# Performance work log

Measured on AMD Instinct MI355X. Metric: run time of the kernel, lower is better.

## Reference

```python
import jax, jax.numpy as jnp
import numpy as np

N = 100000          # num nodes
E = 3200000         # num edges (avg degree 32)
CLIN = 64           # clinical feature dim
MEL_SHAPE = (32, 40)  # flattened -> 1280
MEL = 1280
H = 128             # hidden_dim
C = 4               # num_classes


def setup_inputs() -> dict:
    key = jax.random.key(0)
    ks = jax.random.split(key, 14)
    s = lambda d: 1.0 / np.sqrt(d)
    inp = {
        "clinical": jax.random.normal(ks[0], (N, CLIN), jnp.float32),
        "mel": jax.random.normal(ks[1], (N,) + MEL_SHAPE, jnp.float32),
        "edge_index": jax.random.randint(ks[2], (2, E), 0, N, dtype=jnp.int32),
        # mel_linear
        "Wm": jax.random.normal(ks[3], (H, MEL), jnp.float32) * s(MEL),
        "bm": jnp.zeros((H,), jnp.float32),
        # concat_linear (in = H + CLIN)
        "Wc": jax.random.normal(ks[4], (H, H + CLIN), jnp.float32) * s(H + CLIN),
        "bc": jnp.zeros((H,), jnp.float32),
        # sage1: lin_l (neighbors, with bias), lin_r (root, no bias)
        "Wl1": jax.random.normal(ks[5], (H, H), jnp.float32) * s(H),
        "bl1": jnp.zeros((H,), jnp.float32),
        "Wr1": jax.random.normal(ks[6], (H, H), jnp.float32) * s(H),
        # sage2
        "Wl2": jax.random.normal(ks[7], (C, H), jnp.float32) * s(H),
        "bl2": jnp.zeros((C,), jnp.float32),
        "Wr2": jax.random.normal(ks[8], (C, H), jnp.float32) * s(H),
    }
    return inp


def _sage_conv(x, src, dst, Wl, bl, Wr):
    """PyG SAGEConv with mean aggregation:
    out = lin_l(mean_{j in N(i)} x_j) + lin_r(x_i).
    src = edge_index[0] (message source), dst = edge_index[1] (target).
    """
    msg_sum = jax.ops.segment_sum(x[src], dst, num_segments=N)  # [N, d]
    cnt = jax.ops.segment_sum(jnp.ones((src.shape[0], 1), x.dtype), dst,
                              num_segments=N)                    # [N, 1]
    agg = msg_sum / jnp.maximum(cnt, 1.0)
    return agg @ Wl.T + bl + x @ Wr.T


def reference(clinical, mel, edge_index, Wm, bm, Wc, bc,
              Wl1, bl1, Wr1, Wl2, bl2, Wr2):
    src, dst = edge_index[0], edge_index[1]
    mel_flat = mel.reshape(mel.shape[0], -1)                 # [N, 1280]
    mel_h = jax.nn.relu(mel_flat @ Wm.T + bm)                # [N, H]
    x = jnp.concatenate([clinical, mel_h], axis=1)           # [N, CLIN+H]
    x = jax.nn.relu(x @ Wc.T + bc)                           # [N, H]
    x = jax.nn.relu(_sage_conv(x, src, dst, Wl1, bl1, Wr1))  # [N, H]
    x = _sage_conv(x, src, dst, Wl2, bl2, Wr2)               # [N, C]
    return x
```

## Files before the change

### kernel.cpp

```cpp
#include <hip/hip_runtime.h>
#include <hip/hip_bf16.h>
#include <stdint.h>

#define NN   100000
#define EE   3200000
#define HD   128

typedef short v8s __attribute__((ext_vector_type(8)));
typedef float v4f __attribute__((ext_vector_type(4)));

__device__ __forceinline__ unsigned short f2bf(float f){
  union { float f; unsigned int i; } v; v.f = f;
  unsigned int r = v.i + 0x7fffu + ((v.i >> 16) & 1u);
  return (unsigned short)(r >> 16);
}
__device__ __forceinline__ uint4 pack8(float4 lo, float4 hi){
  uint4 r;
  r.x = (unsigned)f2bf(lo.x) | ((unsigned)f2bf(lo.y) << 16);
  r.y = (unsigned)f2bf(lo.z) | ((unsigned)f2bf(lo.w) << 16);
  r.z = (unsigned)f2bf(hi.x) | ((unsigned)f2bf(hi.y) << 16);
  r.w = (unsigned)f2bf(hi.z) | ((unsigned)f2bf(hi.w) << 16);
  return r;
}

__global__ void k_zero(int* p, int n){
  int i = blockIdx.x*blockDim.x + threadIdx.x; if (i < n) p[i] = 0;
}
__global__ void k_histrank(const int* __restrict__ dst, int* __restrict__ cnt,
                           int* __restrict__ rank, int e){
  int i = blockIdx.x*blockDim.x + threadIdx.x;
  if (i < e) rank[i] = atomicAdd(&cnt[dst[i]], 1);
}
__global__ __launch_bounds__(1024)
void k_scan1(const int* __restrict__ cnt, int* __restrict__ offs, int* __restrict__ blksum, int n){
  __shared__ int lds[1024];
  int t = threadIdx.x; int i = blockIdx.x*1024 + t;
  int v = (i < n) ? cnt[i] : 0;
  lds[t] = v; __syncthreads();
  for (int s = 1; s < 1024; s <<= 1){
    int add = (t >= s) ? lds[t-s] : 0;
    __syncthreads();
    lds[t] += add;
    __syncthreads();
  }
  if (i < n) offs[i] = lds[t] - v;
  if (t == 1023) blksum[blockIdx.x] = lds[1023];
}
__global__ __launch_bounds__(128)
void k_scan2(int* __restrict__ blksum, int nb){
  __shared__ int lds[128];
  int t = threadIdx.x;
  int v = (t < nb) ? blksum[t] : 0;
  lds[t] = v; __syncthreads();
  for (int s = 1; s < 128; s <<= 1){
    int a = (t >= s) ? lds[t-s] : 0;
    __syncthreads();
    lds[t] += a;
    __syncthreads();
  }
  if (t < nb) blksum[t] = lds[t] - v;
}
__global__ __launch_bounds__(1024)
void k_scan3(int* __restrict__ offs, const int* __restrict__ blksum, int n){
  int i = blockIdx.x*1024 + threadIdx.x;
  if (i < n) offs[i] += blksum[blockIdx.x];
}
__global__ void k_place(const int* __restrict__ src, const int* __restrict__ dst,
                        const int* __restrict__ offs, const int* __restrict__ rank,
                        int* __restrict__ ssrc, int e){
  int i = blockIdx.x*blockDim.x + threadIdx.x;
  if (i < e) ssrc[offs[dst[i]] + rank[i]] = src[i];
}

__device__ __forceinline__ void gemm_issue(int t, int T0, int M, int gm, int r0, int c8,
    const void* __restrict__ A0, int lda0, int a0f32,
    const void* __restrict__ A1, int lda1, int a1f32,
    const float* __restrict__ B0, int ldb0,
    const float* __restrict__ B1, int ldb1,
    uint4* as, uint4* bs)
{
  const void* Ag; const float* Bg; int la, lb, ko, af32;
  if (t < T0){ Ag = A0; la = lda0; af32 = a0f32; Bg = B0; lb = ldb0; ko = t*64; }
  else       { Ag = A1; la = lda1; af32 = a1f32; Bg = B1; lb = ldb1; ko = (t-T0)*64; }
#pragma unroll
  for (int p = 0; p < 4; p++){
    int row  = r0 + p*32;
    int grow = gm + row;
    if (grow < M){
      if (af32){
        const float* ap = (const float*)Ag + (size_t)grow*la + ko + c8;
        as[p] = pack8(*(const float4*)ap, *(const float4*)(ap + 4));
      } else {
        as[p] = *(const uint4*)((const unsigned short*)Ag + (size_t)grow*la + ko + c8);
      }
    } else {
      as[p] = make_uint4(0u,0u,0u,0u);
    }
    const float* bp = Bg + (size_t)row*lb + ko + c8;
    bs[p] = pack8(*(const float4*)bp, *(const float4*)(bp + 4));
  }
}

__global__ __launch_bounds__(256)
void k_gemm(int M,
            const void* __restrict__ A0, int lda0, int K0, int a0f32,
            const void* __restrict__ A1, int lda1, int K1, int a1f32,
            const float* __restrict__ B0, int ldb0,
            const float* __restrict__ B1, int ldb1,
            const float* __restrict__ bias, int do_relu,
            unsigned short* __restrict__ C, int ldc)
{
  __shared__ unsigned short Abuf[128*72];
  __shared__ unsigned short Bbuf[128*72];
  const int tid = threadIdx.x;
  const int gm  = blockIdx.x * 128;
  const int T0  = K0 >> 6;
  const int T   = (K0 + K1) >> 6;

  const int r0 = tid >> 3;
  const int c8 = (tid & 7) * 8;

  const int lane = tid & 63;
  const int w  = tid >> 6;
  const int wm = w >> 1, wn = w & 1;
  const int l15 = lane & 15, q = lane >> 4;

  v4f acc[4][4];
#pragma unroll
  for (int mi = 0; mi < 4; mi++)
#pragma unroll
    for (int ni = 0; ni < 4; ni++){ v4f z = {0.f,0.f,0.f,0.f}; acc[mi][ni] = z; }

  uint4 aS[4], bS[4];
  gemm_issue(0, T0, M, gm, r0, c8, A0, lda0, a0f32, A1, lda1, a1f32,
             B0, ldb0, B1, ldb1, aS, bS);

  for (int t = 0; t < T; ++t){
#pragma unroll
    for (int p = 0; p < 4; p++){
      int row = r0 + p*32;
      *(uint4*)(Abuf + row*72 + c8) = aS[p];
      *(uint4*)(Bbuf + row*72 + c8) = bS[p];
    }
    __syncthreads();
    if (t + 1 < T)
      gemm_issue(t+1, T0, M, gm, r0, c8, A0, lda0, a0f32, A1, lda1, a1f32,
                 B0, ldb0, B1, ldb1, aS, bS);
#pragma unroll
    for (int kk = 0; kk < 64; kk += 32){
      v8s af[4], bf[4];
#pragma unroll
      for (int mi = 0; mi < 4; mi++)
        af[mi] = *(const v8s*)(Abuf + (wm*64 + mi*16 + l15)*72 + kk + q*8);
#pragma unroll
      for (int ni = 0; ni < 4; ni++)
        bf[ni] = *(const v8s*)(Bbuf + (wn*64 + ni*16 + l15)*72 + kk + q*8);
#pragma unroll
      for (int mi = 0; mi < 4; mi++)
#pragma unroll
        for (int ni = 0; ni < 4; ni++)
          acc[mi][ni] = __builtin_amdgcn_mfma_f32_16x16x32_bf16(af[mi], bf[ni], acc[mi][ni], 0, 0, 0);
    }
    __syncthreads();
  }

#pragma unroll
  for (int ni = 0; ni < 4; ni++){
    int n = wn*64 + ni*16 + l15;
    float bv = bias ? bias[n] : 0.0f;
#pragma unroll
    for (int mi = 0; mi < 4; mi++){
#pragma unroll
      for (int r = 0; r < 4; r++){
        int row = gm + wm*64 + mi*16 + q*4 + r;
        if (row < M){
          float v = acc[mi][ni][r] + bv;
          if (do_relu) v = v > 0.f ? v : 0.f;
          C[(size_t)row*ldc + n] = f2bf(v);
        }
      }
    }
  }
}

__global__ __launch_bounds__(256)
void k_agg1(const int* __restrict__ offs, const int* __restrict__ cnt,
            const int* __restrict__ ssrc,
            const unsigned short* __restrict__ y1,
            const unsigned short* __restrict__ z1,
            const float* __restrict__ Wl2,
            const float* __restrict__ Wr2,
            const float* __restrict__ bl2,
            float* __restrict__ y2, float* __restrict__ r2, int n)
{
  int wid  = (blockIdx.x * blockDim.x + threadIdx.x) >> 6;
  int lane = threadIdx.x & 63;
  if (wid >= n) return;
  int start = offs[wid];
  int deg   = cnt[wid];
  const unsigned int* y1u = (const unsigned int*)y1;
  float a0 = 0.f, a1 = 0.f;
  for (int base = 0; base < deg; base += 64){
    int idx = base + lane;
    int sl  = (idx < deg) ? ssrc[start + idx] : 0;
    int m   = deg - base; if (m > 64) m = 64;
    for (int t = 0; t < m; ++t){
      int s = __shfl(sl, t, 64);
      unsigned int u = y1u[(size_t)s*64 + lane];
      union {unsigned int i; float f;} lo, hi;
      lo.i = u << 16; hi.i = u & 0xffff0000u;
      a0 += lo.f; a1 += hi.f;
    }
  }
  float scale = 1.0f / (float)(deg > 0 ? deg : 1);
  unsigned int zu = ((const unsigned int*)z1)[(size_t)wid*64 + lane];
  union {unsigned int i; float f;} zl, zh;
  zl.i = zu << 16; zh.i = zu & 0xffff0000u;
  float x0 = a0*scale + zl.f; x0 = x0 > 0.f ? x0 : 0.f;
  float x1 = a1*scale + zh.f; x1 = x1 > 0.f ? x1 : 0.f;

  float pl[4], pr[4];
#pragma unroll
  for (int c = 0; c < 4; c++){
    float2 wl = ((const float2*)Wl2)[c*64 + lane];
    float2 wr = ((const float2*)Wr2)[c*64 + lane];
    pl[c] = x0*wl.x + x1*wl.y;
    pr[c] = x0*wr.x + x1*wr.y;
  }
#pragma unroll
  for (int off = 32; off > 0; off >>= 1){
#pragma unroll
    for (int c = 0; c < 4; c++){
      pl[c] += __shfl_xor(pl[c], off, 64);
      pr[c] += __shfl_xor(pr[c], off, 64);
    }
  }
  if (lane < 4){
    y2[(size_t)wid*4 + lane] = pl[lane];
    r2[(size_t)wid*4 + lane] = pr[lane] + bl2[lane];
  }
}

__global__ void k_agg2(const int* __restrict__ offs, const int* __restrict__ cnt,
                       const int* __restrict__ ssrc,
                       const float* __restrict__ y2, const float* __restrict__ r2,
                       float* __restrict__ out, int n)
{
  int i = blockIdx.x * blockDim.x + threadIdx.x;
  if (i >= n) return;
  int start = offs[i], deg = cnt[i];
  float a0 = 0.f, a1 = 0.f, a2 = 0.f, a3 = 0.f;
  for (int e = 0; e < deg; e++){
    int s = ssrc[start + e];
    float4 v = *(const float4*)(y2 + (size_t)s*4);
    a0 += v.x; a1 += v.y; a2 += v.z; a3 += v.w;
  }
  float sc = 1.0f / (float)(deg > 0 ? deg : 1);
  float4 r = *(const float4*)(r2 + (size_t)i*4);
  float4 o;
  o.x = a0*sc + r.x; o.y = a1*sc + r.y; o.z = a2*sc + r.z; o.w = a3*sc + r.w;
  *(float4*)(out + (size_t)i*4) = o;
}

extern "C" void kernel_launch(void* const* d_in, const int* in_sizes, int n_in,
                              void* d_out, int out_size, void* d_ws, size_t ws_size,
                              hipStream_t stream)
{
  (void)in_sizes; (void)n_in; (void)out_size; (void)ws_size;
  const float* clinical = (const float*)d_in[0];
  const float* mel      = (const float*)d_in[1];
  const int*   ei       = (const int*)d_in[2];
  const float* Wm  = (const float*)d_in[3];
  const float* bm  = (const float*)d_in[4];
  const float* Wc  = (const float*)d_in[5];
  const float* bc  = (const float*)d_in[6];
  const float* Wl1 = (const float*)d_in[7];
  const float* bl1 = (const float*)d_in[8];
  const float* Wr1 = (const float*)d_in[9];
  const float* Wl2 = (const float*)d_in[10];
  const float* bl2 = (const float*)d_in[11];
  const float* Wr2 = (const float*)d_in[12];
  const int* src = ei;
  const int* dst = ei + EE;

  char* w = (char*)d_ws;
  auto alloc = [&](size_t sz){ void* p = (void*)w; w += (sz + 255) & ~(size_t)255; return p; };
  unsigned short* mel_h = (unsigned short*)alloc((size_t)NN*HD*2);
  unsigned short* x     = (unsigned short*)alloc((size_t)NN*HD*2);
  unsigned short* z1    = (unsigned short*)alloc((size_t)NN*HD*2);
  int*   ssrc   = (int*)alloc((size_t)EE*4);
  int*   rank   = (int*)alloc((size_t)EE*4);
  int*   cnt    = (int*)alloc((size_t)NN*4);
  int*   offs   = (int*)alloc((size_t)NN*4);
  int*   blksum = (int*)alloc(4096);
  float* y2     = (float*)alloc((size_t)NN*4*4);
  float* r2     = (float*)alloc((size_t)NN*4*4);

  k_zero<<<(NN+255)/256, 256, 0, stream>>>(cnt, NN);
  k_histrank<<<(EE+255)/256, 256, 0, stream>>>(dst, cnt, rank, EE);
  int nblk = (NN + 1023) / 1024;
  k_scan1<<<nblk, 1024, 0, stream>>>(cnt, offs, blksum, NN);
  k_scan2<<<1, 128, 0, stream>>>(blksum, nblk);
  k_scan3<<<nblk, 1024, 0, stream>>>(offs, blksum, NN);
  k_place<<<(EE+255)/256, 256, 0, stream>>>(src, dst, offs, rank, ssrc, EE);

  int gmb = (NN + 127) / 128;
  k_gemm<<<gmb, 256, 0, stream>>>(NN, mel, 1280, 1280, 1, nullptr, 0, 0, 0,
                                  Wm, 1280, nullptr, 0, bm, 1, mel_h, HD);
  k_gemm<<<gmb, 256, 0, stream>>>(NN, clinical, 64, 64, 1, mel_h, HD, HD, 0,
                                  Wc, 192, Wc + 64, 192, bc, 1, x, HD);
  unsigned short* y1 = mel_h;
  k_gemm<<<gmb, 256, 0, stream>>>(NN, x, HD, HD, 0, nullptr, 0, 0, 0,
                                  Wl1, HD, nullptr, 0, nullptr, 0, y1, HD);
  k_gemm<<<gmb, 256, 0, stream>>>(NN, x, HD, HD, 0, nullptr, 0, 0, 0,
                                  Wr1, HD, nullptr, 0, bl1, 0, z1, HD);

  k_agg1<<<(NN+3)/4, 256, 0, stream>>>(offs, cnt, ssrc, y1, z1, Wl2, Wr2, bl2, y2, r2, NN);
  k_agg2<<<(NN+255)/256, 256, 0, stream>>>(offs, cnt, ssrc, y2, r2, (float*)d_out, NN);
}
```

Baseline: 1.306 ms.

## Gather neighbor rows with 16-byte loads and use wave-per-node second aggregation

```diff
diff --git a/kernel.cpp b/kernel.cpp
--- a/kernel.cpp
+++ b/kernel.cpp
@@ -21,6 +21,17 @@
   r.z = (unsigned)f2bf(hi.x) | ((unsigned)f2bf(hi.y) << 16);
   r.w = (unsigned)f2bf(hi.z) | ((unsigned)f2bf(hi.w) << 16);
   return r;
+}
+__device__ __forceinline__ void acc8(float* a, uint4 u){
+  union {unsigned int i; float f;} t;
+  t.i = u.x << 16;         a[0] += t.f;
+  t.i = u.x & 0xffff0000u; a[1] += t.f;
+  t.i = u.y << 16;         a[2] += t.f;
+  t.i = u.y & 0xffff0000u; a[3] += t.f;
+  t.i = u.z << 16;         a[4] += t.f;
+  t.i = u.z & 0xffff0000u; a[5] += t.f;
+  t.i = u.w << 16;         a[6] += t.f;
+  t.i = u.w & 0xffff0000u; a[7] += t.f;
 }
 
 __global__ void k_zero(int* p, int n){
@@ -198,68 +209,127 @@
   if (wid >= n) return;
   int start = offs[wid];
   int deg   = cnt[wid];
-  const unsigned int* y1u = (const unsigned int*)y1;
-  float a0 = 0.f, a1 = 0.f;
+  const uint4* y1q = (const uint4*)y1;
+  const int g = lane >> 4;
+  const int c = lane & 15;
+
+  float a[8];
+#pragma unroll
+  for (int j = 0; j < 8; j++) a[j] = 0.f;
+
   for (int base = 0; base < deg; base += 64){
     int idx = base + lane;
     int sl  = (idx < deg) ? ssrc[start + idx] : 0;
     int m   = deg - base; if (m > 64) m = 64;
-    for (int t = 0; t < m; ++t){
-      int s = __shfl(sl, t, 64);
-      unsigned int u = y1u[(size_t)s*64 + lane];
-      union {unsigned int i; float f;} lo, hi;
-      lo.i = u << 16; hi.i = u & 0xffff0000u;
-      a0 += lo.f; a1 += hi.f;
-    }
-  }
+    int quads = (m + 3) >> 2;
+    int tq = 0;
+    for (; tq + 2 <= quads; tq += 2){
+      int e0 = tq*4 + g, e1 = e0 + 4;
+      int i0 = e0 < m ? e0 : m-1;
+      int i1 = e1 < m ? e1 : m-1;
+      int s0 = __shfl(sl, i0, 64);
+      int s1 = __shfl(sl, i1, 64);
+      uint4 u0 = y1q[(size_t)s0*16 + c];
+      uint4 u1 = y1q[(size_t)s1*16 + c];
+      if (e0 < m) acc8(a, u0);
+      if (e1 < m) acc8(a, u1);
+    }
+    if (tq < quads){
+      int e0 = tq*4 + g;
+      int i0 = e0 < m ? e0 : m-1;
+      int s0 = __shfl(sl, i0, 64);
+      uint4 u0 = y1q[(size_t)s0*16 + c];
+      if (e0 < m) acc8(a, u0);
+    }
+  }
+#pragma unroll
+  for (int j = 0; j < 8; j++){
+    a[j] += __shfl_xor(a[j], 16, 64);
+    a[j] += __shfl_xor(a[j], 32, 64);
+  }
+
   float scale = 1.0f / (float)(deg > 0 ? deg : 1);
-  unsigned int zu = ((const unsigned int*)z1)[(size_t)wid*64 + lane];
-  union {unsigned int i; float f;} zl, zh;
-  zl.i = zu << 16; zh.i = zu & 0xffff0000u;
-  float x0 = a0*scale + zl.f; x0 = x0 > 0.f ? x0 : 0.f;
-  float x1 = a1*scale + zh.f; x1 = x1 > 0.f ? x1 : 0.f;
+  uint4 zu = ((const uint4*)z1)[(size_t)wid*16 + c];
+  float x8[8];
+  {
+    union {unsigned int i; float f;} t;
+    t.i = zu.x << 16;         x8[0] = t.f;
+    t.i = zu.x & 0xffff0000u; x8[1] = t.f;
+    t.i = zu.y << 16;         x8[2] = t.f;
+    t.i = zu.y & 0xffff0000u; x8[3] = t.f;
+    t.i = zu.z << 16;         x8[4] = t.f;
+    t.i = zu.z & 0xffff0000u; x8[5] = t.f;
+    t.i = zu.w << 16;         x8[6] = t.f;
+    t.i = zu.w & 0xffff0000u; x8[7] = t.f;
+  }
+#pragma unroll
+  for (int j = 0; j < 8; j++){
+    float v = a[j]*scale + x8[j];
+    x8[j] = v > 0.f ? v : 0.f;
+  }
 
   float pl[4], pr[4];
 #pragma unroll
-  for (int c = 0; c < 4; c++){
-    float2 wl = ((const float2*)Wl2)[c*64 + lane];
-    float2 wr = ((const float2*)Wr2)[c*64 + lane];
-    pl[c] = x0*wl.x + x1*wl.y;
-    pr[c] = x0*wr.x + x1*wr.y;
-  }
-#pragma unroll
-  for (int off = 32; off > 0; off >>= 1){
-#pragma unroll
-    for (int c = 0; c < 4; c++){
-      pl[c] += __shfl_xor(pl[c], off, 64);
-      pr[c] += __shfl_xor(pr[c], off, 64);
-    }
-  }
-  if (lane < 4){
-    y2[(size_t)wid*4 + lane] = pl[lane];
-    r2[(size_t)wid*4 + lane] = pr[lane] + bl2[lane];
-  }
-}
-
-__global__ void k_agg2(const int* __restrict__ offs, const int* __restrict__ cnt,
-                       const int* __restrict__ ssrc,
-                       const float* __restrict__ y2, const float* __restrict__ r2,
-                       float* __restrict__ out, int n)
-{
-  int i = blockIdx.x * blockDim.x + threadIdx.x;
-  if (i >= n) return;
-  int start = offs[i], deg = cnt[i];
+  for (int cc = 0; cc < 4; cc++){
+    const float* wl = Wl2 + cc*128 + 8*c;
+    const float* wr = Wr2 + cc*128 + 8*c;
+    float4 wl0 = *(const float4*)wl, wl1 = *(const float4*)(wl + 4);
+    float4 wr0 = *(const float4*)wr, wr1 = *(const float4*)(wr + 4);
+    pl[cc] = x8[0]*wl0.x + x8[1]*wl0.y + x8[2]*wl0.z + x8[3]*wl0.w
+           + x8[4]*wl1.x + x8[5]*wl1.y + x8[6]*wl1.z + x8[7]*wl1.w;
+    pr[cc] = x8[0]*wr0.x + x8[1]*wr0.y + x8[2]*wr0.z + x8[3]*wr0.w
+           + x8[4]*wr1.x + x8[5]*wr1.y + x8[6]*wr1.z + x8[7]*wr1.w;
+  }
+#pragma unroll
+  for (int off = 8; off >= 1; off >>= 1){
+#pragma unroll
+    for (int cc = 0; cc < 4; cc++){
+      pl[cc] += __shfl_xor(pl[cc], off, 64);
+      pr[cc] += __shfl_xor(pr[cc], off, 64);
+    }
+  }
+  if (lane == 0){
+    float4 o; o.x = pl[0]; o.y = pl[1]; o.z = pl[2]; o.w = pl[3];
+    *(float4*)(y2 + (size_t)wid*4) = o;
+    float4 b = *(const float4*)bl2;
+    float4 p; p.x = pr[0]+b.x; p.y = pr[1]+b.y; p.z = pr[2]+b.z; p.w = pr[3]+b.w;
+    *(float4*)(r2 + (size_t)wid*4) = p;
+  }
+}
+
+__global__ __launch_bounds__(256)
+void k_agg2(const int* __restrict__ offs, const int* __restrict__ cnt,
+            const int* __restrict__ ssrc,
+            const float* __restrict__ y2, const float* __restrict__ r2,
+            float* __restrict__ out, int n)
+{
+  int wid  = (blockIdx.x * blockDim.x + threadIdx.x) >> 6;
+  int lane = threadIdx.x & 63;
+  if (wid >= n) return;
+  int start = offs[wid], deg = cnt[wid];
   float a0 = 0.f, a1 = 0.f, a2 = 0.f, a3 = 0.f;
-  for (int e = 0; e < deg; e++){
-    int s = ssrc[start + e];
-    float4 v = *(const float4*)(y2 + (size_t)s*4);
-    a0 += v.x; a1 += v.y; a2 += v.z; a3 += v.w;
-  }
-  float sc = 1.0f / (float)(deg > 0 ? deg : 1);
-  float4 r = *(const float4*)(r2 + (size_t)i*4);
-  float4 o;
-  o.x = a0*sc + r.x; o.y = a1*sc + r.y; o.z = a2*sc + r.z; o.w = a3*sc + r.w;
-  *(float4*)(out + (size_t)i*4) = o;
+  for (int base = 0; base < deg; base += 64){
+    int idx = base + lane;
+    if (idx < deg){
+      int s = ssrc[start + idx];
+      float4 v = *(const float4*)(y2 + (size_t)s*4);
+      a0 += v.x; a1 += v.y; a2 += v.z; a3 += v.w;
+    }
+  }
+#pragma unroll
+  for (int off = 32; off >= 1; off >>= 1){
+    a0 += __shfl_xor(a0, off, 64);
+    a1 += __shfl_xor(a1, off, 64);
+    a2 += __shfl_xor(a2, off, 64);
+    a3 += __shfl_xor(a3, off, 64);
+  }
+  if (lane == 0){
+    float sc = 1.0f / (float)(deg > 0 ? deg : 1);
+    float4 r = *(const float4*)(r2 + (size_t)wid*4);
+    float4 o;
+    o.x = a0*sc + r.x; o.y = a1*sc + r.y; o.z = a2*sc + r.z; o.w = a3*sc + r.w;
+    *(float4*)(out + (size_t)wid*4) = o;
+  }
 }
 
 extern "C" void kernel_launch(void* const* d_in, const int* in_sizes, int n_in,
@@ -316,5 +386,5 @@
                                   Wr1, HD, nullptr, 0, bl1, 0, z1, HD);
 
   k_agg1<<<(NN+3)/4, 256, 0, stream>>>(offs, cnt, ssrc, y1, z1, Wl2, Wr2, bl2, y2, r2, NN);
-  k_agg2<<<(NN+255)/256, 256, 0, stream>>>(offs, cnt, ssrc, y2, r2, (float*)d_out, NN);
-}
+  k_agg2<<<(NN+3)/4, 256, 0, stream>>>(offs, cnt, ssrc, y2, r2, (float*)d_out, NN);
+}
```

New measurement: 1.241 ms. -5.0%, faster.
